# Performance work log

Hardware: AMD Instinct MI355X
Metric: run time of the kernel (lower is better)

Reference implementation:

```python
import jax, jax.numpy as jnp
import numpy as np

B, C, N, K = 8, 64, 4096, 16


def setup_inputs() -> dict:
    key = jax.random.key(0)
    k1, k2 = jax.random.split(key)
    x = jax.random.normal(k1, (B, C, N, 1), dtype=jnp.float32)
    edge_index = jax.random.randint(k2, (B, N, K), 0, N, dtype=jnp.int32)
    alpha = jnp.float32(1.0)  # AlphaLayer parameter, init 1.0
    return {"x": x, "edge_index": edge_index, "alpha": alpha}


def _aggregate_sum(x_nodes, edge_index):
    # x_nodes: [B, N, C]; edge_index: [B, N, K] neighbor ids per node.
    b, n, c = x_nodes.shape
    k = edge_index.shape[-1]
    idx = edge_index.reshape(b, n * k, 1).astype(jnp.int32)
    gathered = jnp.take_along_axis(x_nodes, idx, axis=1)  # [B, N*K, C]
    return gathered.reshape(b, n, k, c).sum(axis=2)       # [B, N, C]


def reference(x, edge_index, alpha):
    # x: [B, C, N, 1] -> permute(0,2,3,1) -> [B, N, 1, C]; W=1 so treat as [B, N, C]
    x_nodes = jnp.transpose(x[..., 0], (0, 2, 1))          # [B, N, C]
    m = _aggregate_sum(x_nodes, edge_index)                # [B, N, C]
    m = jnp.transpose(m, (0, 2, 1))[..., None]             # back to [B, C, N, 1]
    # AlphaLayer: x * (1 + alpha) + m
    return x * (1.0 + alpha) + m
```

## Files before the change

### kernel.cpp

```cpp
#include <hip/hip_runtime.h>

#define B_ 8
#define C_ 64
#define N_ 4096
#define K_ 16
#define THREADS 512
#define NQ 4
#define NODES_PER_BLK (N_ / NQ)
#define NPT (NODES_PER_BLK / THREADS)

__device__ __forceinline__ int slot(int n) { return n ^ ((n >> 3) & 7); }

__global__ __launch_bounds__(THREADS) void fused_k(const float* __restrict__ x,
                                                   const int* __restrict__ ei,
                                                   const float* __restrict__ alpha_p,
                                                   float* __restrict__ out) {
  __shared__ float4 xs[N_];
  const int bid = blockIdx.x;
  const int b   = bid & 7;
  const int cq  = (bid >> 3) & 15;
  const int nq  = bid >> 7;
  const int c0  = cq * 4;
  const int n0  = nq * NODES_PER_BLK;
  const int t   = threadIdx.x;

  int idx[NPT][K_];
  const int* eib = ei + ((size_t)b * N_ + n0) * K_;
#pragma unroll
  for (int q = 0; q < NPT; ++q) {
    const int4* ep = reinterpret_cast<const int4*>(eib + (size_t)(t + q * THREADS) * K_);
    *reinterpret_cast<int4*>(&idx[q][0])  = ep[0];
    *reinterpret_cast<int4*>(&idx[q][4])  = ep[1];
    *reinterpret_cast<int4*>(&idx[q][8])  = ep[2];
    *reinterpret_cast<int4*>(&idx[q][12]) = ep[3];
  }

  const float* xb = x + ((size_t)b * C_ + c0) * N_;
#pragma unroll
  for (int g = 0; g < N_ / (4 * THREADS); ++g) {
    const int j = t + g * THREADS;
    const float4 r0 = *reinterpret_cast<const float4*>(xb + 0 * N_ + 4 * j);
    const float4 r1 = *reinterpret_cast<const float4*>(xb + 1 * N_ + 4 * j);
    const float4 r2 = *reinterpret_cast<const float4*>(xb + 2 * N_ + 4 * j);
    const float4 r3 = *reinterpret_cast<const float4*>(xb + 3 * N_ + 4 * j);
    xs[slot(4 * j + 0)] = make_float4(r0.x, r1.x, r2.x, r3.x);
    xs[slot(4 * j + 1)] = make_float4(r0.y, r1.y, r2.y, r3.y);
    xs[slot(4 * j + 2)] = make_float4(r0.z, r1.z, r2.z, r3.z);
    xs[slot(4 * j + 3)] = make_float4(r0.w, r1.w, r2.w, r3.w);
  }
  __syncthreads();

  const float s = 1.0f + alpha_p[0];
#pragma unroll
  for (int q = 0; q < NPT; ++q) {
    const int n = n0 + t + q * THREADS;
    float4 acc = make_float4(0.f, 0.f, 0.f, 0.f);
#pragma unroll
    for (int k = 0; k < K_; ++k) {
      const float4 v = xs[slot(idx[q][k])];
      acc.x += v.x; acc.y += v.y; acc.z += v.z; acc.w += v.w;
    }
    const float4 sv = xs[slot(n)];
    const size_t o = (size_t)(b * C_ + c0) * N_ + n;
    out[o + 0 * N_] = sv.x * s + acc.x;
    out[o + 1 * N_] = sv.y * s + acc.y;
    out[o + 2 * N_] = sv.z * s + acc.z;
    out[o + 3 * N_] = sv.w * s + acc.w;
  }
}

extern "C" void kernel_launch(void* const* d_in, const int* in_sizes, int n_in,
                              void* d_out, int out_size, void* d_ws, size_t ws_size,
                              hipStream_t stream) {
  const float* x     = (const float*)d_in[0];
  const int*   ei    = (const int*)d_in[1];
  const float* alpha = (const float*)d_in[2];
  float*       out   = (float*)d_out;
  (void)d_ws; (void)ws_size;

  fused_k<<<B_ * (C_ / 4) * NQ, THREADS, 0, stream>>>(x, ei, alpha, out);
}
```

Before: 11.99 us.

## Store node features in shared memory as packed bf16 to halve LDS footprint

Converts the per-block feature table in shared memory from fp32 float4 to packed bf16 (uint2 per node), halving LDS usage so more blocks fit per CU, and raises the launch-bounds occupancy hint. Each thread now handles two adjacent nodes, loads its indices after the barrier, reads the self term in fp32 from global memory and writes float2 outputs. The cost is reduced precision in the neighbor sum and dropping the XOR swizzle, which may add bank conflicts on the 8-byte gathers.

```diff
diff --git a/kernel.cpp b/kernel.cpp
--- a/kernel.cpp
+++ b/kernel.cpp
@@ -1,4 +1,5 @@
 #include <hip/hip_runtime.h>
+#include <hip/hip_bf16.h>
 
 #define B_ 8
 #define C_ 64
@@ -6,66 +7,73 @@
 #define K_ 16
 #define THREADS 512
 #define NQ 4
-#define NODES_PER_BLK (N_ / NQ)
-#define NPT (NODES_PER_BLK / THREADS)
+#define NPB (N_ / NQ)
 
-__device__ __forceinline__ int slot(int n) { return n ^ ((n >> 3) & 7); }
+__device__ __forceinline__ unsigned bfbits(float f) {
+  __hip_bfloat16 h = __float2bfloat16(f);
+  unsigned short u;
+  __builtin_memcpy(&u, &h, sizeof(u));
+  return (unsigned)u;
+}
 
-__global__ __launch_bounds__(THREADS) void fused_k(const float* __restrict__ x,
-                                                   const int* __restrict__ ei,
-                                                   const float* __restrict__ alpha_p,
-                                                   float* __restrict__ out) {
-  __shared__ float4 xs[N_];
+__global__ __launch_bounds__(THREADS, 6) void fused_k(const float* __restrict__ x,
+                                                      const int* __restrict__ ei,
+                                                      const float* __restrict__ alpha_p,
+                                                      float* __restrict__ out) {
+  __shared__ uint2 xs[N_];
   const int bid = blockIdx.x;
   const int b   = bid & 7;
   const int cq  = (bid >> 3) & 15;
   const int nq  = bid >> 7;
   const int c0  = cq * 4;
-  const int n0  = nq * NODES_PER_BLK;
   const int t   = threadIdx.x;
 
-  int idx[NPT][K_];
-  const int* eib = ei + ((size_t)b * N_ + n0) * K_;
+  const float* xb = x + ((size_t)b * C_ + c0) * N_;
+
 #pragma unroll
-  for (int q = 0; q < NPT; ++q) {
-    const int4* ep = reinterpret_cast<const int4*>(eib + (size_t)(t + q * THREADS) * K_);
-    *reinterpret_cast<int4*>(&idx[q][0])  = ep[0];
-    *reinterpret_cast<int4*>(&idx[q][4])  = ep[1];
-    *reinterpret_cast<int4*>(&idx[q][8])  = ep[2];
-    *reinterpret_cast<int4*>(&idx[q][12]) = ep[3];
-  }
-
-  const float* xb = x + ((size_t)b * C_ + c0) * N_;
-#pragma unroll
-  for (int g = 0; g < N_ / (4 * THREADS); ++g) {
+  for (int g = 0; g < N_ / (2 * THREADS); ++g) {
     const int j = t + g * THREADS;
-    const float4 r0 = *reinterpret_cast<const float4*>(xb + 0 * N_ + 4 * j);
-    const float4 r1 = *reinterpret_cast<const float4*>(xb + 1 * N_ + 4 * j);
-    const float4 r2 = *reinterpret_cast<const float4*>(xb + 2 * N_ + 4 * j);
-    const float4 r3 = *reinterpret_cast<const float4*>(xb + 3 * N_ + 4 * j);
-    xs[slot(4 * j + 0)] = make_float4(r0.x, r1.x, r2.x, r3.x);
-    xs[slot(4 * j + 1)] = make_float4(r0.y, r1.y, r2.y, r3.y);
-    xs[slot(4 * j + 2)] = make_float4(r0.z, r1.z, r2.z, r3.z);
-    xs[slot(4 * j + 3)] = make_float4(r0.w, r1.w, r2.w, r3.w);
+    const float2 r0 = *reinterpret_cast<const float2*>(xb + 0 * N_ + 2 * j);
+    const float2 r1 = *reinterpret_cast<const float2*>(xb + 1 * N_ + 2 * j);
+    const float2 r2 = *reinterpret_cast<const float2*>(xb + 2 * N_ + 2 * j);
+    const float2 r3 = *reinterpret_cast<const float2*>(xb + 3 * N_ + 2 * j);
+    uint4 w;
+    w.x = (bfbits(r1.x) << 16) | bfbits(r0.x);
+    w.y = (bfbits(r3.x) << 16) | bfbits(r2.x);
+    w.z = (bfbits(r1.y) << 16) | bfbits(r0.y);
+    w.w = (bfbits(r3.y) << 16) | bfbits(r2.y);
+    *reinterpret_cast<uint4*>(&xs[2 * j]) = w;
   }
   __syncthreads();
 
+  const int n2 = nq * NPB + 2 * t;
+  const int4* ep = reinterpret_cast<const int4*>(ei + ((size_t)b * N_ + n2) * K_);
+  int idx[2][K_];
+#pragma unroll
+  for (int q = 0; q < 8; ++q)
+    *reinterpret_cast<int4*>(&idx[q >> 2][(q & 3) * 4]) = ep[q];
+
+  float acc[2][4] = {{0.f, 0.f, 0.f, 0.f}, {0.f, 0.f, 0.f, 0.f}};
+#pragma unroll
+  for (int p = 0; p < 2; ++p) {
+#pragma unroll
+    for (int k = 0; k < K_; ++k) {
+      const uint2 v = xs[idx[p][k]];
+      acc[p][0] += __uint_as_float(v.x << 16);
+      acc[p][1] += __uint_as_float(v.x & 0xffff0000u);
+      acc[p][2] += __uint_as_float(v.y << 16);
+      acc[p][3] += __uint_as_float(v.y & 0xffff0000u);
+    }
+  }
+
   const float s = 1.0f + alpha_p[0];
 #pragma unroll
-  for (int q = 0; q < NPT; ++q) {
-    const int n = n0 + t + q * THREADS;
-    float4 acc = make_float4(0.f, 0.f, 0.f, 0.f);
-#pragma unroll
-    for (int k = 0; k < K_; ++k) {
-      const float4 v = xs[slot(idx[q][k])];
-      acc.x += v.x; acc.y += v.y; acc.z += v.z; acc.w += v.w;
-    }
-    const float4 sv = xs[slot(n)];
-    const size_t o = (size_t)(b * C_ + c0) * N_ + n;
-    out[o + 0 * N_] = sv.x * s + acc.x;
-    out[o + 1 * N_] = sv.y * s + acc.y;
-    out[o + 2 * N_] = sv.z * s + acc.z;
-    out[o + 3 * N_] = sv.w * s + acc.w;
+  for (int c = 0; c < 4; ++c) {
+    const float2 sv = *reinterpret_cast<const float2*>(xb + c * N_ + n2);
+    float2 ov;
+    ov.x = sv.x * s + acc[0][c];
+    ov.y = sv.y * s + acc[1][c];
+    *reinterpret_cast<float2*>(out + ((size_t)b * C_ + c0 + c) * N_ + n2) = ov;
   }
 }
 
```

Measured after the change: 13.83 us. +15.4%, slower.
